# Kernel tuning notes

Measured on AMD Instinct MI355X. Metric: run time of the kernel, lower is better.

Reference implementation:

```python
import jax, jax.numpy as jnp
import numpy as np

B, S, F, H, D = 32, 512, 32, 8, 300   # batch, seq, n_features, hidden_dim, n_dim_model
FH = min(D, F)                        # flattened GRN hidden = min(n_dim_model, n_features)


def _p(key, shape, scale=0.05):
    return (jax.random.normal(key, shape) * scale).astype(jnp.float32)


def setup_inputs() -> dict:
    key = jax.random.key(0)
    ks = jax.random.split(key, 16)
    return {
        "x": jax.random.normal(ks[0], (B, S, F), dtype=jnp.float32),
        "pre_w": _p(ks[1], (F, H)), "pre_b": _p(ks[2], (F, H)),
        "sg_fc1_w": _p(ks[3], (F, H, H)), "sg_fc1_b": _p(ks[4], (F, H)),
        "sg_fc2_w": _p(ks[5], (F, H, D)), "sg_fc2_b": _p(ks[6], (F, D)),
        "sg_gate_w": _p(ks[7], (F, D, 2 * D)), "sg_gate_b": _p(ks[8], (F, 2 * D)),
        "sg_ln_g": jnp.ones((F, D), jnp.float32), "sg_ln_b": jnp.zeros((F, D), jnp.float32),
        "fl_fc1_w": _p(ks[9], (F * H, FH)), "fl_fc1_b": _p(ks[10], (FH,)),
        "fl_fc2_w": _p(ks[11], (FH, F)), "fl_fc2_b": _p(ks[12], (F,)),
        "fl_gate_w": _p(ks[13], (F, 2 * F)), "fl_gate_b": _p(ks[14], (2 * F,)),
        "fl_ln_g": jnp.ones((F,), jnp.float32), "fl_ln_b": jnp.zeros((F,), jnp.float32),
    }


def _interp_last(x, out_dim):
    # torch F.interpolate(mode='linear', align_corners=True) along the last axis
    in_dim = x.shape[-1]
    pos = jnp.arange(out_dim) * ((in_dim - 1) / (out_dim - 1))
    lo = jnp.floor(pos).astype(jnp.int32)
    hi = jnp.minimum(lo + 1, in_dim - 1)
    w = (pos - lo.astype(pos.dtype)).astype(x.dtype)
    return x[..., lo] * (1 - w) + x[..., hi] * w


def _layer_norm(x, g, b, eps=1e-5):
    m = jnp.mean(x, axis=-1, keepdims=True)
    v = jnp.var(x, axis=-1, keepdims=True)
    return (x - m) * jax.lax.rsqrt(v + eps) * g + b


def _forward(x, pre_w, pre_b, sg_fc1_w, sg_fc1_b, sg_fc2_w, sg_fc2_b,
             sg_gate_w, sg_gate_b, sg_ln_g, sg_ln_b,
             fl_fc1_w, fl_fc1_b, fl_fc2_w, fl_fc2_b, fl_gate_w, fl_gate_b,
             fl_ln_g, fl_ln_b):
    # per-feature prescaler: Linear(1, H) for each of F features, batched
    pre = x[..., None] * pre_w + pre_b                                   # [B,S,F,H]

    # per-feature GRN (H -> H -> D), batched over the feature axis f
    h = jax.nn.elu(jnp.einsum('bsfh,fhk->bsfk', pre, sg_fc1_w) + sg_fc1_b)
    h = jnp.einsum('bsfk,fkd->bsfd', h, sg_fc2_w) + sg_fc2_b             # [B,S,F,D]
    g = jnp.einsum('bsfd,fdp->bsfp', h, sg_gate_w) + sg_gate_b           # [B,S,F,2D]
    glu = g[..., :D] * jax.nn.sigmoid(g[..., D:])
    residual = _interp_last(pre, D)                                      # H -> D interpolate projection
    outputs = _layer_norm(glu + residual, sg_ln_g, sg_ln_b)              # [B,S,F,D]

    # flattened GRN on concatenated prescaler outputs (F*H -> FH -> F)
    flat = pre.reshape(pre.shape[0], pre.shape[1], F * H)                # matches torch.cat order
    fh = jax.nn.elu(flat @ fl_fc1_w + fl_fc1_b)
    fh = fh @ fl_fc2_w + fl_fc2_b                                        # [B,S,F]
    fg = fh @ fl_gate_w + fl_gate_b                                      # [B,S,2F]
    fglu = fg[..., :F] * jax.nn.sigmoid(fg[..., F:])
    wlogits = _layer_norm(fglu + _interp_last(flat, F), fl_ln_g, fl_ln_b)
    w = jax.nn.softmax(wlogits, axis=-1)                                 # [B,S,F]

    out = jnp.einsum('bsfd,bsf->bsd', outputs, w)                        # softmax-weighted sum over features
    return out, w[..., None, :]                                          # weights unsqueezed at dim -2


def reference(x, pre_w, pre_b, sg_fc1_w, sg_fc1_b, sg_fc2_w, sg_fc2_b,
              sg_gate_w, sg_gate_b, sg_ln_g, sg_ln_b,
              fl_fc1_w, fl_fc1_b, fl_fc2_w, fl_fc2_b, fl_gate_w, fl_gate_b,
              fl_ln_g, fl_ln_b):
    return _forward(x, pre_w, pre_b, sg_fc1_w, sg_fc1_b, sg_fc2_w, sg_fc2_b,
                    sg_gate_w, sg_gate_b, sg_ln_g, sg_ln_b,
                    fl_fc1_w, fl_fc1_b, fl_fc2_w, fl_fc2_b, fl_gate_w, fl_gate_b,
                    fl_ln_g, fl_ln_b)
```

## Files before the change

### kernel.cpp

```cpp
#include <hip/hip_runtime.h>
#include <hip/hip_bf16.h>

#define NB 32
#define NS 512
#define NF 32
#define NH 8
#define ND 300
#define NTOK (NB*NS)
#define TPW 4
#define WPB 4
#define TPB (TPW*WPB)

using bf16 = __hip_bfloat16;
typedef float v2f __attribute__((ext_vector_type(2)));

__device__ __forceinline__ float rcpf_(float x){ return __builtin_amdgcn_rcpf(x); }
__device__ __forceinline__ float rsqf_(float x){ return __builtin_amdgcn_rsqf(x); }
__device__ __forceinline__ float sigm(float x){ return rcpf_(1.0f + __expf(-x)); }
__device__ __forceinline__ float eluf(float x){ return x > 0.0f ? x : __expf(x) - 1.0f; }

__device__ __forceinline__ v2f fma2(v2f a, v2f b, v2f c){
    return __builtin_elementwise_fma(a, b, c);
}
__device__ __forceinline__ v2f fma2s(float s, v2f b, v2f c){
    return __builtin_elementwise_fma((v2f){s, s}, b, c);
}

template<int BF16>
__device__ __forceinline__ float ldf(const void* p, size_t i){
    if (BF16) return __bfloat162float(((const bf16*)p)[i]);
    return ((const float*)p)[i];
}
template<int BF16>
__device__ __forceinline__ void stf(void* p, size_t i, float v){
    if (BF16) ((bf16*)p)[i] = __float2bfloat16(v);
    else      ((float*)p)[i] = v;
}

__device__ __forceinline__ bool is_bf16(const void* ones){
    return *(const unsigned*)ones == 0x3F803F80u;
}

template<int CTRL>
__device__ __forceinline__ float dppadd(float v){
    return v + __int_as_float(__builtin_amdgcn_update_dpp(
        0, __float_as_int(v), CTRL, 0xF, 0xF, true));
}
template<int CTRL>
__device__ __forceinline__ float dppmax(float v){
    return fmaxf(v, __int_as_float(__builtin_amdgcn_update_dpp(
        __float_as_int(v), __float_as_int(v), CTRL, 0xF, 0xF, false)));
}
__device__ __forceinline__ float rlane(float v, int l){
    return __int_as_float(__builtin_amdgcn_readlane(__float_as_int(v), l));
}
__device__ __forceinline__ float wsum64(float v){
    v = dppadd<0x111>(v); v = dppadd<0x112>(v); v = dppadd<0x114>(v); v = dppadd<0x118>(v);
    v = dppadd<0x142>(v); v = dppadd<0x143>(v);
    return rlane(v, 63);
}
__device__ __forceinline__ float rsum32(float v){
    v = dppadd<0x111>(v); v = dppadd<0x112>(v); v = dppadd<0x114>(v); v = dppadd<0x118>(v);
    return rlane(v, 15) + rlane(v, 31);
}
__device__ __forceinline__ float rmax32(float v){
    v = dppmax<0x111>(v); v = dppmax<0x112>(v); v = dppmax<0x114>(v); v = dppmax<0x118>(v);
    return fmaxf(rlane(v, 15), rlane(v, 31));
}

template<int BF16>
__device__ void precompute_body(const void* __restrict__ W2, const void* __restrict__ b2,
                                const void* __restrict__ Wg, const void* __restrict__ bg,
                                const void* __restrict__ sg_g, const void* __restrict__ sg_b,
                                float* __restrict__ Crow,
                                float (*part)[64][10], float (*w2s)[2400], float (*b2s)[300])
{
    const int tid = threadIdx.x;
    const int l = tid & 63;
    const int q = tid >> 6;
    const int fj = blockIdx.x * 64 + l;
    const int f = fj / 600;
    const int j = fj % 600;

    const int fLo = (blockIdx.x * 64) / 600;
    const int fHi = (blockIdx.x * 64 + 63) / 600;

    for (int ff = 0; ff <= fHi - fLo; ++ff) {
        for (int idx = tid; idx < 2400; idx += 256)
            w2s[ff][idx] = ldf<BF16>(W2, (size_t)(fLo + ff) * 2400 + idx);
        for (int idx = tid; idx < 300; idx += 256)
            b2s[ff][idx] = ldf<BF16>(b2, (size_t)(fLo + ff) * 300 + idx);
    }
    __syncthreads();

    const float* myW2 = w2s[f - fLo];
    const float* myB2 = b2s[f - fLo];
    const size_t WgBase = (size_t)f * 180000 + j;

    float acc[8] = {0,0,0,0,0,0,0,0};
    float accb = 0.f;
    for (int m = q * 75; m < q * 75 + 75; ++m) {
        float wg = ldf<BF16>(Wg, WgBase + (size_t)m * 600);
        #pragma unroll
        for (int k = 0; k < 8; ++k)
            acc[k] += myW2[k * 300 + m] * wg;
        accb += myB2[m] * wg;
    }
    #pragma unroll
    for (int k = 0; k < 8; ++k) part[q][l][k] = acc[k];
    part[q][l][8] = accb;
    __syncthreads();

    const int d = (j < 300) ? j : j - 300;
    const int half = (j < 300) ? 0 : 1;
    float* row = Crow + ((size_t)f * 300 + d) * 20;
    for (int v = q; v < 9; v += 4) {
        float s = part[0][l][v] + part[1][l][v] + part[2][l][v] + part[3][l][v];
        if (v < 8) {
            row[2 * v + half] = s;
        } else {
            float bc = s + ldf<BF16>(bg, (size_t)f * 600 + j);
            if (j < 300) {
                row[16] = bc;
                row[18] = ldf<BF16>(sg_g, (size_t)f * 300 + d);
                row[19] = ldf<BF16>(sg_b, (size_t)f * 300 + d);
            } else {
                row[17] = bc;
            }
        }
    }
}

__global__ void precompute_kernel(const void* __restrict__ W2, const void* __restrict__ b2,
                                  const void* __restrict__ Wg, const void* __restrict__ bg,
                                  const void* __restrict__ sg_g, const void* __restrict__ sg_b,
                                  float* __restrict__ Crow)
{
    __shared__ float part[4][64][10];
    __shared__ float w2s[2][2400];
    __shared__ float b2s[2][300];
    if (is_bf16(sg_g))
        precompute_body<1>(W2, b2, Wg, bg, sg_g, sg_b, Crow, part, w2s, b2s);
    else
        precompute_body<0>(W2, b2, Wg, bg, sg_g, sg_b, Crow, part, w2s, b2s);
}

template<int BF16>
__device__ void vsn_body(const void* __restrict__ x,
                         const void* __restrict__ pre_w, const void* __restrict__ pre_b,
                         const void* __restrict__ W1,    const void* __restrict__ b1,
                         const void* __restrict__ fl1w,  const void* __restrict__ fl1b,
                         const void* __restrict__ fl2w,  const void* __restrict__ fl2b,
                         const void* __restrict__ flgw,  const void* __restrict__ flgb,
                         const void* __restrict__ flng,  const void* __restrict__ flnb,
                         const float* __restrict__ Crow,
                         void* __restrict__ d_out, float* preS_, float* hS_)
{
    void* outMain = d_out;
    void* outW    = (char*)d_out + (size_t)NTOK * ND * (BF16 ? 2 : 4);

    const int tid  = threadIdx.x;
    const int wave = tid >> 6;
    const int lane = tid & 63;
    const int tokBase = blockIdx.x * TPB + wave * TPW;

    float* myPre = preS_ + wave * (TPW * 256);
    float* myH   = hS_   + wave * (TPW * 256);

    {
        float pw[4], pb[4];
        #pragma unroll
        for (int q = 0; q < 4; ++q) {
            pw[q] = ldf<BF16>(pre_w, 4 * lane + q);
            pb[q] = ldf<BF16>(pre_b, 4 * lane + q);
        }
        const int fidx = lane >> 1;
        #pragma unroll
        for (int t = 0; t < TPW; ++t) {
            float xv = ldf<BF16>(x, (size_t)(tokBase + t) * NF + fidx);
            float4 v;
            v.x = xv * pw[0] + pb[0];
            v.y = xv * pw[1] + pb[1];
            v.z = xv * pw[2] + pb[2];
            v.w = xv * pw[3] + pb[3];
            *(float4*)(&myPre[t * 256 + 4 * lane]) = v;
        }
    }

    {
        const int f  = lane >> 1;
        const int kh = (lane & 1) * 4;
        float w1r[8][4], b1r[4];
        #pragma unroll
        for (int m = 0; m < 8; ++m)
            #pragma unroll
            for (int q = 0; q < 4; ++q)
                w1r[m][q] = ldf<BF16>(W1, (size_t)(f * 8 + m) * 8 + kh + q);
        #pragma unroll
        for (int q = 0; q < 4; ++q) b1r[q] = ldf<BF16>(b1, f * 8 + kh + q);

        #pragma unroll
        for (int t = 0; t < TPW; ++t) {
            float pr[8];
            float4 pA = *(const float4*)(&myPre[t * 256 + f * 8]);
            float4 pB = *(const float4*)(&myPre[t * 256 + f * 8 + 4]);
            pr[0]=pA.x; pr[1]=pA.y; pr[2]=pA.z; pr[3]=pA.w;
            pr[4]=pB.x; pr[5]=pB.y; pr[6]=pB.z; pr[7]=pB.w;
            float a[4] = {b1r[0], b1r[1], b1r[2], b1r[3]};
            #pragma unroll
            for (int m = 0; m < 8; ++m)
                #pragma unroll
                for (int q = 0; q < 4; ++q)
                    a[q] += pr[m] * w1r[m][q];
            float4 hv4;
            hv4.x = eluf(a[0]); hv4.y = eluf(a[1]); hv4.z = eluf(a[2]); hv4.w = eluf(a[3]);
            *(float4*)(&myH[t * 256 + 4 * lane]) = hv4;
        }
    }

    const int jj = lane & 31;
    const int hB = lane >> 5;
    float wreg[TPW];
    {
        float f1b = (hB == 0) ? ldf<BF16>(fl1b, jj) : 0.0f;
        v2f p1a = {f1b, f1b};
        v2f p1c = {f1b, f1b};
        for (int kg = 0; kg < 32; ++kg) {
            const int kk = hB * 128 + kg * 4;
            float4 pr0 = *(const float4*)(&myPre[0 * 256 + kk]);
            float4 pr1 = *(const float4*)(&myPre[1 * 256 + kk]);
            float4 pr2 = *(const float4*)(&myPre[2 * 256 + kk]);
            float4 pr3 = *(const float4*)(&myPre[3 * 256 + kk]);
            float w0 = ldf<BF16>(fl1w, (size_t)(kk + 0) * 32 + jj);
            float w1 = ldf<BF16>(fl1w, (size_t)(kk + 1) * 32 + jj);
            float w2 = ldf<BF16>(fl1w, (size_t)(kk + 2) * 32 + jj);
            float w3 = ldf<BF16>(fl1w, (size_t)(kk + 3) * 32 + jj);
            p1a = fma2((v2f){pr0.x, pr1.x}, (v2f){w0, w0}, p1a);
            p1c = fma2((v2f){pr2.x, pr3.x}, (v2f){w0, w0}, p1c);
            p1a = fma2((v2f){pr0.y, pr1.y}, (v2f){w1, w1}, p1a);
            p1c = fma2((v2f){pr2.y, pr3.y}, (v2f){w1, w1}, p1c);
            p1a = fma2((v2f){pr0.z, pr1.z}, (v2f){w2, w2}, p1a);
            p1c = fma2((v2f){pr2.z, pr3.z}, (v2f){w2, w2}, p1c);
            p1a = fma2((v2f){pr0.w, pr1.w}, (v2f){w3, w3}, p1a);
            p1c = fma2((v2f){pr2.w, pr3.w}, (v2f){w3, w3}, p1c);
        }
        float p1[TPW] = {p1a.x, p1a.y, p1c.x, p1c.y};
        float fhv[TPW];
        #pragma unroll
        for (int t = 0; t < TPW; ++t)
            fhv[t] = eluf(p1[t] + __shfl_xor(p1[t], 32));

        float p2[TPW];
        float f2b = ldf<BF16>(fl2b, jj);
        #pragma unroll
        for (int t = 0; t < TPW; ++t) p2[t] = f2b;
        #pragma unroll
        for (int k = 0; k < 32; ++k) {
            float wv = ldf<BF16>(fl2w, k * 32 + jj);
            #pragma unroll
            for (int t = 0; t < TPW; ++t) p2[t] += rlane(fhv[t], k) * wv;
        }
        float p3[TPW];
        float fgbv = ldf<BF16>(flgb, lane);
        #pragma unroll
        for (int t = 0; t < TPW; ++t) p3[t] = fgbv;
        #pragma unroll
        for (int k = 0; k < 32; ++k) {
            float wv = ldf<BF16>(flgw, k * 64 + lane);
            #pragma unroll
            for (int t = 0; t < TPW; ++t) p3[t] += rlane(p2[t], k) * wv;
        }

        float lng = ldf<BF16>(flng, jj), lnb = ldf<BF16>(flnb, jj);
        float posB = (float)jj * (255.0f / 31.0f);
        int loB = (int)floorf(posB); loB = loB < 0 ? 0 : (loB > 254 ? 254 : loB);
        float frB = posB - (float)loB;

        #pragma unroll
        for (int t = 0; t < TPW; ++t) {
            float fgA  = __shfl(p3[t], jj);
            float fgB  = __shfl(p3[t], jj + 32);
            float fglu = fgA * sigm(fgB);
            float pl = myPre[t * 256 + loB];
            float ph = myPre[t * 256 + loB + 1];
            float tv = fglu + pl + frB * (ph - pl);
            float S1 = rsum32(tv);
            float S2 = rsum32(tv * tv);
            float mean = S1 * (1.0f / 32.0f);
            float var  = fmaxf(S2 * (1.0f / 32.0f) - mean * mean, 0.0f);
            float rs   = rsqf_(var + 1e-5f);
            float wl   = (tv - mean) * rs * lng + lnb;
            float mx   = rmax32(wl);
            float e    = __expf(wl - mx);
            float ss   = rsum32(e);
            float wv   = e * rcpf_(ss);
            wreg[t] = wv;
            if (lane < 32) stf<BF16>(outW, (size_t)(tokBase + t) * NF + lane, wv);
        }
    }

    int lo_[5]; float fr_[5];
    #pragma unroll
    for (int i = 0; i < 5; ++i) {
        int d = i * 64 + lane;
        float pos = (float)d * (7.0f / 299.0f);
        int lo = (int)floorf(pos); lo = lo < 0 ? 0 : (lo > 6 ? 6 : lo);
        lo_[i] = lo; fr_[i] = pos - (float)lo;
    }

    float acc[TPW][5];
    #pragma unroll
    for (int t = 0; t < TPW; ++t)
        #pragma unroll
        for (int i = 0; i < 5; ++i) acc[t][i] = 0.0f;

    for (int f = 0; f < NF; ++f) {
        float hv[TPW][8];
        #pragma unroll
        for (int t = 0; t < TPW; ++t) {
            float4 h0 = *(const float4*)(&myH[t * 256 + f * 8]);
            float4 h1 = *(const float4*)(&myH[t * 256 + f * 8 + 4]);
            hv[t][0]=h0.x; hv[t][1]=h0.y; hv[t][2]=h0.z; hv[t][3]=h0.w;
            hv[t][4]=h1.x; hv[t][5]=h1.y; hv[t][6]=h1.z; hv[t][7]=h1.w;
        }

        float tt[TPW][5], s1[TPW], s2[TPW], lgv[5], lbv[5];
        #pragma unroll
        for (int t = 0; t < TPW; ++t) { s1[t] = 0.0f; s2[t] = 0.0f; }

        #pragma unroll
        for (int i = 0; i < 5; ++i) {
            int d = i * 64 + lane;
            bool ok = (d < ND);
            const float4* row = (const float4*)(Crow + ((size_t)f * ND + (ok ? d : ND - 1)) * 20);
            float4 q0 = row[0], q1 = row[1], q2 = row[2], q3 = row[3], ex = row[4];
            v2f P0 = {q0.x, q0.y}, P1 = {q0.z, q0.w};
            v2f P2 = {q1.x, q1.y}, P3 = {q1.z, q1.w};
            v2f P4 = {q2.x, q2.y}, P5 = {q2.z, q2.w};
            v2f P6 = {q3.x, q3.y}, P7 = {q3.z, q3.w};
            lgv[i] = ex.z; lbv[i] = ex.w;
            int base = f * 8 + lo_[i];
            #pragma unroll
            for (int t = 0; t < TPW; ++t) {
                const float* h = hv[t];
                v2f g = {ex.x, ex.y};
                g = fma2s(h[0], P0, g);
                g = fma2s(h[1], P1, g);
                g = fma2s(h[2], P2, g);
                g = fma2s(h[3], P3, g);
                g = fma2s(h[4], P4, g);
                g = fma2s(h[5], P5, g);
                g = fma2s(h[6], P6, g);
                g = fma2s(h[7], P7, g);
                float pl = myPre[t * 256 + base];
                float ph = myPre[t * 256 + base + 1];
                float tv = g.x * sigm(g.y) + pl + fr_[i] * (ph - pl);
                tv = ok ? tv : 0.0f;
                tt[t][i] = tv; s1[t] += tv; s2[t] += tv * tv;
            }
        }

        #pragma unroll
        for (int t = 0; t < TPW; ++t) {
            float S1 = wsum64(s1[t]);
            float S2 = wsum64(s2[t]);
            float mean = S1 * (1.0f / 300.0f);
            float var  = fmaxf(S2 * (1.0f / 300.0f) - mean * mean, 0.0f);
            float rs   = rsqf_(var + 1e-5f);
            float wf   = rlane(wreg[t], f);
            float wrs  = wf * rs;
            #pragma unroll
            for (int i = 0; i < 5; ++i) {
                int d = i * 64 + lane;
                if (d < ND) {
                    float a = wrs * lgv[i];
                    acc[t][i] += a * tt[t][i] + (wf * lbv[i] - a * mean);
                }
            }
        }
    }

    #pragma unroll
    for (int t = 0; t < TPW; ++t) {
        const size_t tok = (size_t)tokBase + t;
        #pragma unroll
        for (int i = 0; i < 5; ++i) {
            int d = i * 64 + lane;
            if (d < ND) stf<BF16>(outMain, tok * ND + d, acc[t][i]);
        }
    }
}

__launch_bounds__(256)
__global__ void vsn_main(const void* __restrict__ x,
                         const void* __restrict__ pre_w, const void* __restrict__ pre_b,
                         const void* __restrict__ W1,    const void* __restrict__ b1,
                         const void* __restrict__ fl1w,  const void* __restrict__ fl1b,
                         const void* __restrict__ fl2w,  const void* __restrict__ fl2b,
                         const void* __restrict__ flgw,  const void* __restrict__ flgb,
                         const void* __restrict__ flng,  const void* __restrict__ flnb,
                         const float* __restrict__ Crow, void* __restrict__ d_out)
{
    __shared__ float preS_[WPB * TPW * 256];
    __shared__ float hS_[WPB * TPW * 256];
    if (is_bf16(flng))
        vsn_body<1>(x, pre_w, pre_b, W1, b1, fl1w, fl1b, fl2w, fl2b,
                    flgw, flgb, flng, flnb, Crow, d_out, preS_, hS_);
    else
        vsn_body<0>(x, pre_w, pre_b, W1, b1, fl1w, fl1b, fl2w, fl2b,
                    flgw, flgb, flng, flnb, Crow, d_out, preS_, hS_);
}

extern "C" void kernel_launch(void* const* d_in, const int* in_sizes, int n_in,
                              void* d_out, int out_size, void* d_ws, size_t ws_size,
                              hipStream_t stream)
{
    const void* x     = d_in[0];
    const void* pre_w = d_in[1];
    const void* pre_b = d_in[2];
    const void* W1    = d_in[3];
    const void* b1    = d_in[4];
    const void* W2    = d_in[5];
    const void* b2    = d_in[6];
    const void* Wg    = d_in[7];
    const void* bg    = d_in[8];
    const void* sg_g  = d_in[9];
    const void* sg_b  = d_in[10];
    const void* fl1w  = d_in[11];
    const void* fl1b  = d_in[12];
    const void* fl2w  = d_in[13];
    const void* fl2b  = d_in[14];
    const void* flgw  = d_in[15];
    const void* flgb  = d_in[16];
    const void* flng  = d_in[17];
    const void* flnb  = d_in[18];

    float* Crow = (float*)d_ws;

    precompute_kernel<<<300, 256, 0, stream>>>(W2, b2, Wg, bg, sg_g, sg_b, Crow);

    vsn_main<<<NTOK / TPB, 256, 0, stream>>>(x, pre_w, pre_b, W1, b1,
        fl1w, fl1b, fl2w, fl2b, flgw, flgb, flng, flnb, Crow, d_out);
}
```

Before: 328.5 us.

## Pack folded GRN weights as bf16 and double tokens per wave

Precompute now emits, for each (feature, d) row, the eight folded FC2·gate weight pairs packed as bf16 pairs plus fp32 biases and LayerNorm params. Each row is 48 bytes instead of 80, and precompute uses half as many blocks, each computing both gate halves. The main kernel processes 8 tokens per wave instead of 4 and loads the Crow rows once per feature, reusing them across all tokens to cut repeated global loads. The trade-off is bf16 rounding of the folded weights, which adds numeric error, and more shared memory and registers per block, which can lower occupancy.

```diff
diff --git a/kernel.cpp b/kernel.cpp
--- a/kernel.cpp
+++ b/kernel.cpp
@@ -7,7 +7,7 @@
 #define NH 8
 #define ND 300
 #define NTOK (NB*NS)
-#define TPW 4
+#define TPW 8
 #define WPB 4
 #define TPB (TPW*WPB)
 
@@ -41,6 +41,15 @@
     return *(const unsigned*)ones == 0x3F803F80u;
 }
 
+__device__ __forceinline__ v2f unpk(unsigned u){
+    return (v2f){ __int_as_float((int)(u << 16)),
+                  __int_as_float((int)(u & 0xFFFF0000u)) };
+}
+__device__ __forceinline__ unsigned pack_bf(float a, float b){
+    bf16 ha = __float2bfloat16(a), hb = __float2bfloat16(b);
+    return (unsigned)*(unsigned short*)&ha | ((unsigned)*(unsigned short*)&hb << 16);
+}
+
 template<int CTRL>
 __device__ __forceinline__ float dppadd(float v){
     return v + __int_as_float(__builtin_amdgcn_update_dpp(
@@ -72,18 +81,18 @@
 __device__ void precompute_body(const void* __restrict__ W2, const void* __restrict__ b2,
                                 const void* __restrict__ Wg, const void* __restrict__ bg,
                                 const void* __restrict__ sg_g, const void* __restrict__ sg_b,
-                                float* __restrict__ Crow,
-                                float (*part)[64][10], float (*w2s)[2400], float (*b2s)[300])
+                                unsigned* __restrict__ Crow,
+                                float (*part)[64][18], float (*w2s)[2400], float (*b2s)[300])
 {
     const int tid = threadIdx.x;
     const int l = tid & 63;
     const int q = tid >> 6;
-    const int fj = blockIdx.x * 64 + l;
-    const int f = fj / 600;
-    const int j = fj % 600;
-
-    const int fLo = (blockIdx.x * 64) / 600;
-    const int fHi = (blockIdx.x * 64 + 63) / 600;
+    const int fd = blockIdx.x * 64 + l;
+    const int f = fd / 300;
+    const int d = fd % 300;
+
+    const int fLo = (blockIdx.x * 64) / 300;
+    const int fHi = (blockIdx.x * 64 + 63) / 300;
 
     for (int ff = 0; ff <= fHi - fLo; ++ff) {
         for (int idx = tid; idx < 2400; idx += 256)
@@ -95,38 +104,47 @@
 
     const float* myW2 = w2s[f - fLo];
     const float* myB2 = b2s[f - fLo];
-    const size_t WgBase = (size_t)f * 180000 + j;
-
-    float acc[8] = {0,0,0,0,0,0,0,0};
-    float accb = 0.f;
+    const size_t WgA = (size_t)f * 180000 + d;
+
+    float accA[8] = {0,0,0,0,0,0,0,0};
+    float accB[8] = {0,0,0,0,0,0,0,0};
+    float bA = 0.f, bB = 0.f;
     for (int m = q * 75; m < q * 75 + 75; ++m) {
-        float wg = ldf<BF16>(Wg, WgBase + (size_t)m * 600);
-        #pragma unroll
-        for (int k = 0; k < 8; ++k)
-            acc[k] += myW2[k * 300 + m] * wg;
-        accb += myB2[m] * wg;
+        float wa = ldf<BF16>(Wg, WgA + (size_t)m * 600);
+        float wb = ldf<BF16>(Wg, WgA + (size_t)m * 600 + 300);
+        #pragma unroll
+        for (int k = 0; k < 8; ++k) {
+            float w2v = myW2[k * 300 + m];
+            accA[k] += w2v * wa;
+            accB[k] += w2v * wb;
+        }
+        bA += myB2[m] * wa;
+        bB += myB2[m] * wb;
     }
     #pragma unroll
-    for (int k = 0; k < 8; ++k) part[q][l][k] = acc[k];
-    part[q][l][8] = accb;
+    for (int k = 0; k < 8; ++k) { part[q][l][k] = accA[k]; part[q][l][8 + k] = accB[k]; }
+    part[q][l][16] = bA;
+    part[q][l][17] = bB;
     __syncthreads();
 
-    const int d = (j < 300) ? j : j - 300;
-    const int half = (j < 300) ? 0 : 1;
-    float* row = Crow + ((size_t)f * 300 + d) * 20;
-    for (int v = q; v < 9; v += 4) {
-        float s = part[0][l][v] + part[1][l][v] + part[2][l][v] + part[3][l][v];
+    unsigned* row = Crow + (size_t)fd * 12;
+    for (int v = q; v < 12; v += 4) {
         if (v < 8) {
-            row[2 * v + half] = s;
+            float sA = part[0][l][v] + part[1][l][v] + part[2][l][v] + part[3][l][v];
+            float sB = part[0][l][8+v] + part[1][l][8+v] + part[2][l][8+v] + part[3][l][8+v];
+            row[v] = pack_bf(sA, sB);
+        } else if (v == 8) {
+            float s = part[0][l][16] + part[1][l][16] + part[2][l][16] + part[3][l][16];
+            float bc = s + ldf<BF16>(bg, (size_t)f * 600 + d);
+            row[8] = __float_as_uint(bc);
+        } else if (v == 9) {
+            float s = part[0][l][17] + part[1][l][17] + part[2][l][17] + part[3][l][17];
+            float bc = s + ldf<BF16>(bg, (size_t)f * 600 + d + 300);
+            row[9] = __float_as_uint(bc);
+        } else if (v == 10) {
+            row[10] = __float_as_uint(ldf<BF16>(sg_g, (size_t)f * 300 + d));
         } else {
-            float bc = s + ldf<BF16>(bg, (size_t)f * 600 + j);
-            if (j < 300) {
-                row[16] = bc;
-                row[18] = ldf<BF16>(sg_g, (size_t)f * 300 + d);
-                row[19] = ldf<BF16>(sg_b, (size_t)f * 300 + d);
-            } else {
-                row[17] = bc;
-            }
+            row[11] = __float_as_uint(ldf<BF16>(sg_b, (size_t)f * 300 + d));
         }
     }
 }
@@ -134,9 +152,9 @@
 __global__ void precompute_kernel(const void* __restrict__ W2, const void* __restrict__ b2,
                                   const void* __restrict__ Wg, const void* __restrict__ bg,
                                   const void* __restrict__ sg_g, const void* __restrict__ sg_b,
-                                  float* __restrict__ Crow)
+                                  unsigned* __restrict__ Crow)
 {
-    __shared__ float part[4][64][10];
+    __shared__ float part[4][64][18];
     __shared__ float w2s[2][2400];
     __shared__ float b2s[2][300];
     if (is_bf16(sg_g))
@@ -153,7 +171,7 @@
                          const void* __restrict__ fl2w,  const void* __restrict__ fl2b,
                          const void* __restrict__ flgw,  const void* __restrict__ flgb,
                          const void* __restrict__ flng,  const void* __restrict__ flnb,
-                         const float* __restrict__ Crow,
+                         const unsigned* __restrict__ Crow,
                          void* __restrict__ d_out, float* preS_, float* hS_)
 {
     void* outMain = d_out;
@@ -223,32 +241,33 @@
     float wreg[TPW];
     {
         float f1b = (hB == 0) ? ldf<BF16>(fl1b, jj) : 0.0f;
-        v2f p1a = {f1b, f1b};
-        v2f p1c = {f1b, f1b};
+        v2f p1v[4];
+        #pragma unroll
+        for (int g = 0; g < 4; ++g) p1v[g] = (v2f){f1b, f1b};
         for (int kg = 0; kg < 32; ++kg) {
             const int kk = hB * 128 + kg * 4;
-            float4 pr0 = *(const float4*)(&myPre[0 * 256 + kk]);
-            float4 pr1 = *(const float4*)(&myPre[1 * 256 + kk]);
-            float4 pr2 = *(const float4*)(&myPre[2 * 256 + kk]);
-            float4 pr3 = *(const float4*)(&myPre[3 * 256 + kk]);
+            float4 pr[TPW];
+            #pragma unroll
+            for (int t = 0; t < TPW; ++t)
+                pr[t] = *(const float4*)(&myPre[t * 256 + kk]);
             float w0 = ldf<BF16>(fl1w, (size_t)(kk + 0) * 32 + jj);
             float w1 = ldf<BF16>(fl1w, (size_t)(kk + 1) * 32 + jj);
             float w2 = ldf<BF16>(fl1w, (size_t)(kk + 2) * 32 + jj);
             float w3 = ldf<BF16>(fl1w, (size_t)(kk + 3) * 32 + jj);
-            p1a = fma2((v2f){pr0.x, pr1.x}, (v2f){w0, w0}, p1a);
-            p1c = fma2((v2f){pr2.x, pr3.x}, (v2f){w0, w0}, p1c);
-            p1a = fma2((v2f){pr0.y, pr1.y}, (v2f){w1, w1}, p1a);
-            p1c = fma2((v2f){pr2.y, pr3.y}, (v2f){w1, w1}, p1c);
-            p1a = fma2((v2f){pr0.z, pr1.z}, (v2f){w2, w2}, p1a);
-            p1c = fma2((v2f){pr2.z, pr3.z}, (v2f){w2, w2}, p1c);
-            p1a = fma2((v2f){pr0.w, pr1.w}, (v2f){w3, w3}, p1a);
-            p1c = fma2((v2f){pr2.w, pr3.w}, (v2f){w3, w3}, p1c);
-        }
-        float p1[TPW] = {p1a.x, p1a.y, p1c.x, p1c.y};
+            #pragma unroll
+            for (int g = 0; g < 4; ++g) {
+                p1v[g] = fma2((v2f){pr[2*g].x, pr[2*g+1].x}, (v2f){w0, w0}, p1v[g]);
+                p1v[g] = fma2((v2f){pr[2*g].y, pr[2*g+1].y}, (v2f){w1, w1}, p1v[g]);
+                p1v[g] = fma2((v2f){pr[2*g].z, pr[2*g+1].z}, (v2f){w2, w2}, p1v[g]);
+                p1v[g] = fma2((v2f){pr[2*g].w, pr[2*g+1].w}, (v2f){w3, w3}, p1v[g]);
+            }
+        }
         float fhv[TPW];
         #pragma unroll
-        for (int t = 0; t < TPW; ++t)
-            fhv[t] = eluf(p1[t] + __shfl_xor(p1[t], 32));
+        for (int t = 0; t < TPW; ++t) {
+            float p1 = (t & 1) ? p1v[t >> 1].y : p1v[t >> 1].x;
+            fhv[t] = eluf(p1 + __shfl_xor(p1, 32));
+        }
 
         float p2[TPW];
         float f2b = ldf<BF16>(fl2b, jj);
@@ -315,55 +334,56 @@
         for (int i = 0; i < 5; ++i) acc[t][i] = 0.0f;
 
     for (int f = 0; f < NF; ++f) {
-        float hv[TPW][8];
-        #pragma unroll
-        for (int t = 0; t < TPW; ++t) {
-            float4 h0 = *(const float4*)(&myH[t * 256 + f * 8]);
-            float4 h1 = *(const float4*)(&myH[t * 256 + f * 8 + 4]);
-            hv[t][0]=h0.x; hv[t][1]=h0.y; hv[t][2]=h0.z; hv[t][3]=h0.w;
-            hv[t][4]=h1.x; hv[t][5]=h1.y; hv[t][6]=h1.z; hv[t][7]=h1.w;
-        }
-
-        float tt[TPW][5], s1[TPW], s2[TPW], lgv[5], lbv[5];
-        #pragma unroll
-        for (int t = 0; t < TPW; ++t) { s1[t] = 0.0f; s2[t] = 0.0f; }
-
+        v2f  P[5][8];
+        float bcA[5], bcB[5], lgv[5], lbv[5];
         #pragma unroll
         for (int i = 0; i < 5; ++i) {
             int d = i * 64 + lane;
             bool ok = (d < ND);
-            const float4* row = (const float4*)(Crow + ((size_t)f * ND + (ok ? d : ND - 1)) * 20);
-            float4 q0 = row[0], q1 = row[1], q2 = row[2], q3 = row[3], ex = row[4];
-            v2f P0 = {q0.x, q0.y}, P1 = {q0.z, q0.w};
-            v2f P2 = {q1.x, q1.y}, P3 = {q1.z, q1.w};
-            v2f P4 = {q2.x, q2.y}, P5 = {q2.z, q2.w};
-            v2f P6 = {q3.x, q3.y}, P7 = {q3.z, q3.w};
-            lgv[i] = ex.z; lbv[i] = ex.w;
-            int base = f * 8 + lo_[i];
-            #pragma unroll
-            for (int t = 0; t < TPW; ++t) {
-                const float* h = hv[t];
-                v2f g = {ex.x, ex.y};
-                g = fma2s(h[0], P0, g);
-                g = fma2s(h[1], P1, g);
-                g = fma2s(h[2], P2, g);
-                g = fma2s(h[3], P3, g);
-                g = fma2s(h[4], P4, g);
-                g = fma2s(h[5], P5, g);
-                g = fma2s(h[6], P6, g);
-                g = fma2s(h[7], P7, g);
+            const uint4* row = (const uint4*)(Crow + ((size_t)f * ND + (ok ? d : ND - 1)) * 12);
+            uint4 c0 = row[0], c1 = row[1], c2 = row[2];
+            P[i][0] = unpk(c0.x); P[i][1] = unpk(c0.y);
+            P[i][2] = unpk(c0.z); P[i][3] = unpk(c0.w);
+            P[i][4] = unpk(c1.x); P[i][5] = unpk(c1.y);
+            P[i][6] = unpk(c1.z); P[i][7] = unpk(c1.w);
+            bcA[i] = __uint_as_float(c2.x);
+            bcB[i] = __uint_as_float(c2.y);
+            lgv[i] = __uint_as_float(c2.z);
+            lbv[i] = __uint_as_float(c2.w);
+        }
+
+        #pragma unroll
+        for (int t = 0; t < TPW; ++t) {
+            float h[8];
+            float4 h0 = *(const float4*)(&myH[t * 256 + f * 8]);
+            float4 h1 = *(const float4*)(&myH[t * 256 + f * 8 + 4]);
+            h[0]=h0.x; h[1]=h0.y; h[2]=h0.z; h[3]=h0.w;
+            h[4]=h1.x; h[5]=h1.y; h[6]=h1.z; h[7]=h1.w;
+
+            float tt[5], a1 = 0.f, a2 = 0.f;
+            #pragma unroll
+            for (int i = 0; i < 5; ++i) {
+                int d = i * 64 + lane;
+                bool ok = (d < ND);
+                v2f g = {bcA[i], bcB[i]};
+                g = fma2s(h[0], P[i][0], g);
+                g = fma2s(h[1], P[i][1], g);
+                g = fma2s(h[2], P[i][2], g);
+                g = fma2s(h[3], P[i][3], g);
+                g = fma2s(h[4], P[i][4], g);
+                g = fma2s(h[5], P[i][5], g);
+                g = fma2s(h[6], P[i][6], g);
+                g = fma2s(h[7], P[i][7], g);
+                int base = f * 8 + lo_[i];
                 float pl = myPre[t * 256 + base];
                 float ph = myPre[t * 256 + base + 1];
                 float tv = g.x * sigm(g.y) + pl + fr_[i] * (ph - pl);
                 tv = ok ? tv : 0.0f;
-                tt[t][i] = tv; s1[t] += tv; s2[t] += tv * tv;
+                tt[i] = tv; a1 += tv; a2 += tv * tv;
             }
-        }
-
-        #pragma unroll
-        for (int t = 0; t < TPW; ++t) {
-            float S1 = wsum64(s1[t]);
-            float S2 = wsum64(s2[t]);
+
+            float S1 = wsum64(a1);
+            float S2 = wsum64(a2);
             float mean = S1 * (1.0f / 300.0f);
             float var  = fmaxf(S2 * (1.0f / 300.0f) - mean * mean, 0.0f);
             float rs   = rsqf_(var + 1e-5f);
@@ -374,7 +394,7 @@
                 int d = i * 64 + lane;
                 if (d < ND) {
                     float a = wrs * lgv[i];
-                    acc[t][i] += a * tt[t][i] + (wf * lbv[i] - a * mean);
+                    acc[t][i] += a * tt[i] + (wf * lbv[i] - a * mean);
                 }
             }
         }
@@ -399,7 +419,7 @@
                          const void* __restrict__ fl2w,  const void* __restrict__ fl2b,
                          const void* __restrict__ flgw,  const void* __restrict__ flgb,
                          const void* __restrict__ flng,  const void* __restrict__ flnb,
-                         const float* __restrict__ Crow, void* __restrict__ d_out)
+                         const unsigned* __restrict__ Crow, void* __restrict__ d_out)
 {
     __shared__ float preS_[WPB * TPW * 256];
     __shared__ float hS_[WPB * TPW * 256];
@@ -435,9 +455,9 @@
     const void* flng  = d_in[17];
     const void* flnb  = d_in[18];
 
-    float* Crow = (float*)d_ws;
-
-    precompute_kernel<<<300, 256, 0, stream>>>(W2, b2, Wg, bg, sg_g, sg_b, Crow);
+    unsigned* Crow = (unsigned*)d_ws;
+
+    precompute_kernel<<<150, 256, 0, stream>>>(W2, b2, Wg, bg, sg_g, sg_b, Crow);
 
     vsn_main<<<NTOK / TPB, 256, 0, stream>>>(x, pre_w, pre_b, W1, b1,
         fl1w, fl1b, fl2w, fl2b, flgw, flgb, flng, flnb, Crow, d_out);
```

Measured after the change: 322.6 us. About the same (-1.8%).
